# Performance work log

Hardware: AMD Instinct MI355X
Metric: run time of the kernel (lower is better)

## Reference

```python
import jax, jax.numpy as jnp
import numpy as np

SIZE = 128
DELTA = 1.0
NUM_SHELLS = SIZE // 2  # 64 shells up to Nyquist; corners beyond Nyquist are discarded
DROP_DC = False
ALPHA = None
EPS = 1e-8


def _make_shell_idx(n, delta):
    # integer-frequency radial coordinate, same grid as torch.fft.fftfreq(n)*n
    f = np.fft.fftfreq(n) * n
    fx, fy, fz = np.meshgrid(f, f, f, indexing="ij")
    r = np.sqrt(fx * fx + fy * fy + fz * fz)
    idx = np.floor(r / delta).astype(np.int32)
    # voxels past the Nyquist shell go to a discard bucket (index NUM_SHELLS)
    idx = np.where(idx < NUM_SHELLS, idx, NUM_SHELLS)
    return idx


def setup_inputs() -> dict:
    key = jax.random.key(0)
    k1, k2 = jax.random.split(key)
    shape = (8, 1, SIZE, SIZE, SIZE)
    img_ref = jax.random.normal(k1, shape, dtype=jnp.float32)
    img_pred = jax.random.normal(k2, shape, dtype=jnp.float32)
    shell_idx = jnp.asarray(_make_shell_idx(SIZE, DELTA))
    return {"img_ref": img_ref, "img_pred": img_pred, "shell_idx": shell_idx}


def reference(img_ref, img_pred, shell_idx):
    B = img_ref.shape[0] * img_ref.shape[1]
    V = SIZE * SIZE * SIZE
    F1 = jnp.fft.fftn(img_ref, axes=(-3, -2, -1)).reshape(B, V)
    F2 = jnp.fft.fftn(img_pred, axes=(-3, -2, -1)).reshape(B, V)
    idx = shell_idx.reshape(V)

    # per-shell reductions (single pass, replaces num_shells dense mask-multiplies)
    cross = (F1 * jnp.conj(F2)).real          # Re sum F1 conj(F2) per shell
    p1 = (F1.real ** 2 + F1.imag ** 2)
    p2 = (F2.real ** 2 + F2.imag ** 2)

    seg = jax.vmap(lambda x: jax.ops.segment_sum(x, idx, num_segments=NUM_SHELLS + 1))
    num = seg(cross)[:, :NUM_SHELLS]          # [B, num_shells], drop discard bucket
    d1 = seg(p1)[:, :NUM_SHELLS]
    d2 = seg(p2)[:, :NUM_SHELLS]

    fsc = num / (jnp.sqrt(d1 * d2) + EPS)     # [B, num_shells]

    if ALPHA is not None:
        freq = (jnp.arange(NUM_SHELLS, dtype=jnp.float32) + 0.5) * DELTA / SIZE
        fsc = fsc * (freq ** ALPHA)
    if DROP_DC:
        fsc = fsc[:, 1:]

    loss = 1.0 - jnp.mean(fsc ** 2)
    return loss
```

## Files before the change

kernel.cpp:

```cpp
#include <hip/hip_runtime.h>
#include <math.h>

#define N      128
#define LOGN   7
#define NSQ    (N * N)
#define VOL    (N * N * N)
#define NSHELL 64
#define BTOT   8
#define FPI    3.14159265358979323846f

#define TL     16
#define TP     (TL + 1)

__device__ inline float2* fft16(float2* A, float2* B, int t) {
    const int j5 = t & 31;
    const int lg = (t >> 5) << 1;
    float2* src = A;
    float2* dst = B;
#pragma unroll
    for (int s = 0; s < 6; s += 2) {
        const int Ns = 1 << s;
        const int m  = j5 & (Ns - 1);
        const int cc = j5 >> s;
        const int e0 = (cc << (s + 2)) + m;
        float s2, c2;
        __sincosf(-FPI * (float)m / (float)(2 * Ns), &s2, &c2);
        const float cw = c2 * c2 - s2 * s2;
        const float sw = 2.f * c2 * s2;
        __syncthreads();
#pragma unroll
        for (int l = 0; l < 2; ++l) {
            const int line = lg + l;
            const float2 a  = src[ j5       * TP + line];
            const float2 cv = src[(j5 + 32) * TP + line];
            const float2 b  = src[(j5 + 64) * TP + line];
            const float2 d  = src[(j5 + 96) * TP + line];
            const float wbx = b.x * cw - b.y * sw, wby = b.x * sw + b.y * cw;
            const float wdx = d.x * cw - d.y * sw, wdy = d.x * sw + d.y * cw;
            const float Apx = a.x + wbx, Apy = a.y + wby;
            const float Amx = a.x - wbx, Amy = a.y - wby;
            const float Bpx = cv.x + wdx, Bpy = cv.y + wdy;
            const float Bmx = cv.x - wdx, Bmy = cv.y - wdy;
            const float t0x = Bpx * c2 - Bpy * s2, t0y = Bpx * s2 + Bpy * c2;
            const float t1x = Bmx * c2 - Bmy * s2, t1y = Bmx * s2 + Bmy * c2;
            dst[(e0)          * TP + line] = make_float2(Apx + t0x, Apy + t0y);
            dst[(e0 + Ns)     * TP + line] = make_float2(Amx + t1y, Amy - t1x);
            dst[(e0 + 2 * Ns) * TP + line] = make_float2(Apx - t0x, Apy - t0y);
            dst[(e0 + 3 * Ns) * TP + line] = make_float2(Amx - t1y, Amy + t1x);
        }
        float2* tmp = src; src = dst; dst = tmp;
    }
    {
        const int m   = t & 63;
        const int grp = (t >> 6) << 2;
        float sw, cw;
        __sincosf(-FPI * (float)m / 64.f, &sw, &cw);
        __syncthreads();
#pragma unroll
        for (int l = 0; l < 4; ++l) {
            const int line = grp + l;
            const float2 v0 = src[m * TP + line];
            const float2 v1 = src[(m + 64) * TP + line];
            const float wx = v1.x * cw - v1.y * sw;
            const float wy = v1.x * sw + v1.y * cw;
            dst[m * TP + line]        = make_float2(v0.x + wx, v0.y + wy);
            dst[(m + 64) * TP + line] = make_float2(v0.x - wx, v0.y - wy);
        }
    }
    __syncthreads();
    return dst;
}

__global__ __launch_bounds__(256) void k_fftz_pack(const float* __restrict__ ref,
                                                   const float* __restrict__ pred,
                                                   float2* __restrict__ Z, int b0) {
    __shared__ float2 A[N * TP], B[N * TP];
    const int t  = threadIdx.x;
    const int yt = blockIdx.x & 7;
    const int x  = (blockIdx.x >> 3) & (N - 1);
    const int bl = blockIdx.x >> 10;
    const size_t inbase = (size_t)(b0 + bl) * VOL + (size_t)x * NSQ + (size_t)yt * TL * N;
    const size_t zbase  = (size_t)bl * VOL + (size_t)x * NSQ + (size_t)yt * TL * N;
#pragma unroll
    for (int i = 0; i < 8; ++i) {
        const int elem = i * 256 + t;
        const int z = elem & (N - 1);
        const int j = elem >> LOGN;
        A[z * TP + j] = make_float2(ref[inbase + elem], pred[inbase + elem]);
    }
    float2* res = fft16(A, B, t);
#pragma unroll
    for (int i = 0; i < 8; ++i) {
        const int elem = i * 256 + t;
        const int z = elem & (N - 1);
        const int j = elem >> LOGN;
        Z[zbase + elem] = res[z * TP + j];
    }
}

__global__ __launch_bounds__(256) void k_fft_strided(float2* __restrict__ Z,
                                                     int stride, int midmul) {
    __shared__ float2 A[N * TP], B[N * TP];
    const int t   = threadIdx.x;
    const int zt  = blockIdx.x & 7;
    const int mid = (blockIdx.x >> 3) & (N - 1);
    const int bl  = blockIdx.x >> 10;
    const size_t base = (size_t)bl * VOL + (size_t)mid * midmul + (size_t)zt * TL;
#pragma unroll
    for (int i = 0; i < 8; ++i) {
        const int elem = i * 256 + t;
        const int zz = elem & (TL - 1);
        const int j  = elem >> 4;
        A[j * TP + zz] = Z[base + (size_t)j * stride + zz];
    }
    float2* res = fft16(A, B, t);
#pragma unroll
    for (int i = 0; i < 8; ++i) {
        const int elem = i * 256 + t;
        const int zz = elem & (TL - 1);
        const int j  = elem >> 4;
        Z[base + (size_t)j * stride + zz] = res[j * TP + zz];
    }
}

__device__ inline int isqrt_i(int r2) {
    int s = (int)sqrtf((float)r2);
    s -= (s * s > r2);
    s += ((s + 1) * (s + 1) <= r2);
    return s;
}

__global__ __launch_bounds__(256) void k_reduce(const float2* __restrict__ Z,
                                                float* __restrict__ accum, int b0) {
    const int tid = threadIdx.x;
    const int bl  = blockIdx.x >> 9;
    const int x   = (blockIdx.x >> 2) & (N - 1);
    const int y0  = (blockIdx.x & 3) * 16;
    const int z   = tid & (N - 1);
    const int ys  = (tid >> 7) * 8;

    const int fx = x - ((x >= 64) ? N : 0);
    const int fz = z - ((z >= 64) ? N : 0);

    if (fx * fx + y0 * y0 >= 4096) return;

    __shared__ float sh[4 * 193];
    for (int i = tid; i < 4 * 193; i += 256) sh[i] = 0.f;
    __syncthreads();

    const int mx = (N - x) & (N - 1);
    const int mz = (N - z) & (N - 1);
    const size_t zb = (size_t)bl * VOL;
    const float2* Ap = Z + zb + (size_t)x  * NSQ + z;
    const float2* Bp = Z + zb + (size_t)mx * NSQ + mz;

    float* bins = sh + (tid & 3) * 193;
    const int fxx = fx * fx;
    const int fzz = fz * fz;

    float aC = 0.f, aP1 = 0.f, aP2 = 0.f;
    int cs = -1;
#pragma unroll
    for (int j = 0; j < 8; ++j) {
        const int y  = y0 + ys + j;
        const int s  = isqrt_i(fxx + y * y + fzz);
        if (s != cs) {
            if (cs >= 0 && cs < NSHELL) {
                atomicAdd(&bins[cs * 3 + 0], aC);
                atomicAdd(&bins[cs * 3 + 1], aP1);
                atomicAdd(&bins[cs * 3 + 2], aP2);
            }
            cs = s; aC = 0.f; aP1 = 0.f; aP2 = 0.f;
        }
        if (s < NSHELL) {
            const float w = (y == 0) ? 1.f : 2.f;
            const int my = (N - y) & (N - 1);
            const float2 Av = Ap[(size_t)y  * N];
            const float2 Bv = Bp[(size_t)my * N];
            const float F1x = 0.5f * (Av.x + Bv.x);
            const float F1y = 0.5f * (Av.y - Bv.y);
            const float F2x = 0.5f * (Av.y + Bv.y);
            const float F2y = 0.5f * (Bv.x - Av.x);
            aC  += w * (F1x * F2x + F1y * F2y);
            aP1 += w * (F1x * F1x + F1y * F1y);
            aP2 += w * (F2x * F2x + F2y * F2y);
        }
    }
    if (cs >= 0 && cs < NSHELL) {
        atomicAdd(&bins[cs * 3 + 0], aC);
        atomicAdd(&bins[cs * 3 + 1], aP1);
        atomicAdd(&bins[cs * 3 + 2], aP2);
    }
    __syncthreads();

    float* acc = accum + (size_t)(b0 + bl) * (NSHELL * 3);
    for (int i = tid; i < NSHELL * 3; i += 256) {
        const float v = sh[i] + sh[193 + i] + sh[2 * 193 + i] + sh[3 * 193 + i];
        atomicAdd(&acc[i], v);
    }
}

__global__ __launch_bounds__(512) void k_final(const float* __restrict__ accum,
                                               float* __restrict__ out) {
    __shared__ float red[8];
    const int tid = threadIdx.x;
    const float* a = accum + (size_t)tid * 3;
    const float fsc = a[0] / (sqrtf(a[1] * a[2]) + 1e-8f);
    float v = fsc * fsc;
#pragma unroll
    for (int off = 32; off > 0; off >>= 1) v += __shfl_down(v, off);
    if ((tid & 63) == 0) red[tid >> 6] = v;
    __syncthreads();
    if (tid == 0) {
        float ssum = 0.f;
#pragma unroll
        for (int i = 0; i < 8; ++i) ssum += red[i];
        out[0] = 1.0f - ssum / 512.0f;
    }
}

extern "C" void kernel_launch(void* const* d_in, const int* in_sizes, int n_in,
                              void* d_out, int out_size, void* d_ws, size_t ws_size,
                              hipStream_t stream) {
    const float* ref  = (const float*)d_in[0];
    const float* pred = (const float*)d_in[1];
    float* out = (float*)d_out;

    char*   ws    = (char*)d_ws;
    float*  accum = (float*)ws;
    float2* Zbuf  = (float2*)(ws + 8192);

    const size_t zbytes = (size_t)VOL * sizeof(float2);
    int cap = 1;
    if (ws_size > 8192) {
        size_t c = (ws_size - 8192) / zbytes;
        cap = (c < 1) ? 1 : (c > BTOT ? BTOT : (int)c);
    }

    hipMemsetAsync(accum, 0, BTOT * NSHELL * 3 * sizeof(float), stream);

    for (int b0 = 0; b0 < BTOT; b0 += cap) {
        const int nb = (BTOT - b0 < cap) ? (BTOT - b0) : cap;
        const int nblk = nb * 1024;
        k_fftz_pack<<<nblk, 256, 0, stream>>>(ref, pred, Zbuf, b0);
        k_fft_strided<<<nblk, 256, 0, stream>>>(Zbuf, N, NSQ);
        k_fft_strided<<<nblk, 256, 0, stream>>>(Zbuf, NSQ, N);
        k_reduce<<<nb * 512, 256, 0, stream>>>(Zbuf, accum, b0);
    }
    k_final<<<1, 512, 0, stream>>>(accum, out);
}
```

Baseline: 309.4 us.

## Fuse z/y FFTs per plane and x-FFT into shell reduction using wave shuffles

Replaces the shared-memory radix-4 FFT pipeline (three FFT kernels plus a reduction kernel) with two kernels. The first does the z and y FFTs of a whole x-plane, using wavefront shuffle-based 128-point FFTs with bit-reversed stores through an on-chip plane buffer. The second does the x-axis FFT and the shell reduction together, with no intermediate global write. This removes two full read/write passes over the complex volume and the extra launches. In exchange it needs large shared-memory tiles and 1024-thread blocks, and it reorganises the symmetry handling (full y range, no weight factor), which lowers occupancy and changes the amount of reduction work.

```diff
diff --git a/kernel.cpp b/kernel.cpp
--- a/kernel.cpp
+++ b/kernel.cpp
@@ -2,124 +2,83 @@
 #include <math.h>
 
 #define N      128
-#define LOGN   7
 #define NSQ    (N * N)
 #define VOL    (N * N * N)
 #define NSHELL 64
 #define BTOT   8
 #define FPI    3.14159265358979323846f
 
-#define TL     16
-#define TP     (TL + 1)
-
-__device__ inline float2* fft16(float2* A, float2* B, int t) {
-    const int j5 = t & 31;
-    const int lg = (t >> 5) << 1;
-    float2* src = A;
-    float2* dst = B;
-#pragma unroll
-    for (int s = 0; s < 6; s += 2) {
-        const int Ns = 1 << s;
-        const int m  = j5 & (Ns - 1);
-        const int cc = j5 >> s;
-        const int e0 = (cc << (s + 2)) + m;
-        float s2, c2;
-        __sincosf(-FPI * (float)m / (float)(2 * Ns), &s2, &c2);
-        const float cw = c2 * c2 - s2 * s2;
-        const float sw = 2.f * c2 * s2;
-        __syncthreads();
-#pragma unroll
-        for (int l = 0; l < 2; ++l) {
-            const int line = lg + l;
-            const float2 a  = src[ j5       * TP + line];
-            const float2 cv = src[(j5 + 32) * TP + line];
-            const float2 b  = src[(j5 + 64) * TP + line];
-            const float2 d  = src[(j5 + 96) * TP + line];
-            const float wbx = b.x * cw - b.y * sw, wby = b.x * sw + b.y * cw;
-            const float wdx = d.x * cw - d.y * sw, wdy = d.x * sw + d.y * cw;
-            const float Apx = a.x + wbx, Apy = a.y + wby;
-            const float Amx = a.x - wbx, Amy = a.y - wby;
-            const float Bpx = cv.x + wdx, Bpy = cv.y + wdy;
-            const float Bmx = cv.x - wdx, Bmy = cv.y - wdy;
-            const float t0x = Bpx * c2 - Bpy * s2, t0y = Bpx * s2 + Bpy * c2;
-            const float t1x = Bmx * c2 - Bmy * s2, t1y = Bmx * s2 + Bmy * c2;
-            dst[(e0)          * TP + line] = make_float2(Apx + t0x, Apy + t0y);
-            dst[(e0 + Ns)     * TP + line] = make_float2(Amx + t1y, Amy - t1x);
-            dst[(e0 + 2 * Ns) * TP + line] = make_float2(Apx - t0x, Apy - t0y);
-            dst[(e0 + 3 * Ns) * TP + line] = make_float2(Amx - t1y, Amy + t1x);
-        }
-        float2* tmp = src; src = dst; dst = tmp;
-    }
+#define PP     130
+#define TP2    17
+
+__device__ inline void mk_tw(int l, float* tc, float* ts, float* te) {
+    __sincosf(-FPI * (float)l * (1.0f / 64.0f), &ts[0], &tc[0]);
+#pragma unroll
+    for (int k = 1; k <= 6; ++k) {
+        const int h = 64 >> k;
+        float s, c;
+        __sincosf(-FPI * (float)(l & (h - 1)) / (float)h, &s, &c);
+        const bool hi = (l & h) != 0;
+        tc[k] = hi ? c : 1.0f;
+        ts[k] = hi ? s : 0.0f;
+        te[k] = hi ? -1.0f : 1.0f;
+    }
+}
+
+__device__ inline void fft128(float2& v0, float2& v1,
+                              const float* tc, const float* ts, const float* te) {
     {
-        const int m   = t & 63;
-        const int grp = (t >> 6) << 2;
-        float sw, cw;
-        __sincosf(-FPI * (float)m / 64.f, &sw, &cw);
-        __syncthreads();
-#pragma unroll
-        for (int l = 0; l < 4; ++l) {
-            const int line = grp + l;
-            const float2 v0 = src[m * TP + line];
-            const float2 v1 = src[(m + 64) * TP + line];
-            const float wx = v1.x * cw - v1.y * sw;
-            const float wy = v1.x * sw + v1.y * cw;
-            dst[m * TP + line]        = make_float2(v0.x + wx, v0.y + wy);
-            dst[(m + 64) * TP + line] = make_float2(v0.x - wx, v0.y - wy);
-        }
-    }
-    __syncthreads();
-    return dst;
-}
-
-__global__ __launch_bounds__(256) void k_fftz_pack(const float* __restrict__ ref,
-                                                   const float* __restrict__ pred,
-                                                   float2* __restrict__ Z, int b0) {
-    __shared__ float2 A[N * TP], B[N * TP];
-    const int t  = threadIdx.x;
-    const int yt = blockIdx.x & 7;
-    const int x  = (blockIdx.x >> 3) & (N - 1);
-    const int bl = blockIdx.x >> 10;
-    const size_t inbase = (size_t)(b0 + bl) * VOL + (size_t)x * NSQ + (size_t)yt * TL * N;
-    const size_t zbase  = (size_t)bl * VOL + (size_t)x * NSQ + (size_t)yt * TL * N;
-#pragma unroll
-    for (int i = 0; i < 8; ++i) {
-        const int elem = i * 256 + t;
-        const int z = elem & (N - 1);
-        const int j = elem >> LOGN;
-        A[z * TP + j] = make_float2(ref[inbase + elem], pred[inbase + elem]);
-    }
-    float2* res = fft16(A, B, t);
-#pragma unroll
-    for (int i = 0; i < 8; ++i) {
-        const int elem = i * 256 + t;
-        const int z = elem & (N - 1);
-        const int j = elem >> LOGN;
-        Z[zbase + elem] = res[z * TP + j];
-    }
-}
-
-__global__ __launch_bounds__(256) void k_fft_strided(float2* __restrict__ Z,
-                                                     int stride, int midmul) {
-    __shared__ float2 A[N * TP], B[N * TP];
-    const int t   = threadIdx.x;
-    const int zt  = blockIdx.x & 7;
-    const int mid = (blockIdx.x >> 3) & (N - 1);
-    const int bl  = blockIdx.x >> 10;
-    const size_t base = (size_t)bl * VOL + (size_t)mid * midmul + (size_t)zt * TL;
-#pragma unroll
-    for (int i = 0; i < 8; ++i) {
-        const int elem = i * 256 + t;
-        const int zz = elem & (TL - 1);
-        const int j  = elem >> 4;
-        A[j * TP + zz] = Z[base + (size_t)j * stride + zz];
-    }
-    float2* res = fft16(A, B, t);
-#pragma unroll
-    for (int i = 0; i < 8; ++i) {
-        const int elem = i * 256 + t;
-        const int zz = elem & (TL - 1);
-        const int j  = elem >> 4;
-        Z[base + (size_t)j * stride + zz] = res[j * TP + zz];
+        const float dx = v0.x - v1.x, dy = v0.y - v1.y;
+        v0.x += v1.x; v0.y += v1.y;
+        v1.x = dx * tc[0] - dy * ts[0];
+        v1.y = dx * ts[0] + dy * tc[0];
+    }
+#pragma unroll
+    for (int k = 1; k <= 6; ++k) {
+        const int h = 64 >> k;
+        const float c = tc[k], s = ts[k], e = te[k];
+        const float o0x = __shfl_xor(v0.x, h), o0y = __shfl_xor(v0.y, h);
+        const float o1x = __shfl_xor(v1.x, h), o1y = __shfl_xor(v1.y, h);
+        const float t0x = fmaf(e, v0.x, o0x), t0y = fmaf(e, v0.y, o0y);
+        const float t1x = fmaf(e, v1.x, o1x), t1y = fmaf(e, v1.y, o1y);
+        v0.x = t0x * c - t0y * s;  v0.y = t0x * s + t0y * c;
+        v1.x = t1x * c - t1y * s;  v1.y = t1x * s + t1y * c;
+    }
+}
+
+__global__ __launch_bounds__(1024) void k_fft_zy(const float* __restrict__ ref,
+                                                 const float* __restrict__ pred,
+                                                 float2* __restrict__ Z, int b0) {
+    __shared__ __align__(16) float2 plane[N * PP];
+    const int t = threadIdx.x, l = t & 63, w = t >> 6;
+    const int x  = blockIdx.x & (N - 1);
+    const int bl = blockIdx.x >> 7;
+    float tc[7], ts[7], te[7];
+    mk_tw(l, tc, ts, te);
+    const int f2 = (int)(__brev((unsigned)l) >> 26) << 1;
+
+    const size_t inb = (size_t)(b0 + bl) * VOL + (size_t)x * NSQ;
+#pragma unroll 2
+    for (int k = 0; k < 8; ++k) {
+        const int y = w * 8 + k;
+        const float* rp = ref  + inb + (size_t)y * N;
+        const float* pp = pred + inb + (size_t)y * N;
+        float2 v0 = make_float2(rp[l],      pp[l]);
+        float2 v1 = make_float2(rp[l + 64], pp[l + 64]);
+        fft128(v0, v1, tc, ts, te);
+        *reinterpret_cast<float4*>(&plane[y * PP + f2]) =
+            make_float4(v0.x, v0.y, v1.x, v1.y);
+    }
+    __syncthreads();
+    const size_t zb = (size_t)bl * VOL + (size_t)x * NSQ;
+#pragma unroll 2
+    for (int k = 0; k < 8; ++k) {
+        const int z = w * 8 + k;
+        float2 v0 = plane[l * PP + z];
+        float2 v1 = plane[(l + 64) * PP + z];
+        fft128(v0, v1, tc, ts, te);
+        *reinterpret_cast<float4*>(&Z[zb + (size_t)z * N + f2]) =
+            make_float4(v0.x, v0.y, v1.x, v1.y);
     }
 }
 
@@ -130,72 +89,96 @@
     return s;
 }
 
-__global__ __launch_bounds__(256) void k_reduce(const float2* __restrict__ Z,
-                                                float* __restrict__ accum, int b0) {
-    const int tid = threadIdx.x;
-    const int bl  = blockIdx.x >> 9;
-    const int x   = (blockIdx.x >> 2) & (N - 1);
-    const int y0  = (blockIdx.x & 3) * 16;
-    const int z   = tid & (N - 1);
-    const int ys  = (tid >> 7) * 8;
-
+__global__ __launch_bounds__(512, 4) void k_fftx_reduce(const float2* __restrict__ Z,
+                                                        float* __restrict__ accum, int b0) {
+    const int t = threadIdx.x, l = t & 63, w = t >> 6;
+    const int yt = blockIdx.x & 7;
+    const int z  = (blockIdx.x >> 3) & (N - 1);
+    const int bl = blockIdx.x >> 10;
+    const int fz = z - ((z >= 64) ? N : 0);
+    const int minfy = (yt < 4) ? yt * 16 : 113 - yt * 16;
+    if (fz * fz + minfy * minfy >= NSHELL * NSHELL) return;
+
+    __shared__ __align__(16) float2 TT[2 * N * TP2];
+    __shared__ float bins[4 * 193];
+    const int NT = N * TP2;
+
+    const int mz = (N - z) & (N - 1);
+    const size_t zbA = (size_t)bl * VOL + (size_t)z  * N;
+    const size_t zbB = (size_t)bl * VOL + (size_t)mz * N;
+#pragma unroll
+    for (int k = 0; k < 4; ++k) {
+        const int e  = k * 512 + t;
+        const int xx = e >> 4, yi = e & 15;
+        const int y  = yt * 16 + yi;
+        const int my = (N - y) & (N - 1);
+        TT[xx * TP2 + yi]      = Z[zbA + (size_t)xx * NSQ + y];
+        TT[NT + xx * TP2 + yi] = Z[zbB + (size_t)xx * NSQ + my];
+    }
+    for (int i = t; i < 4 * 193; i += 512) bins[i] = 0.f;
+
+    float tc[7], ts[7], te[7];
+    mk_tw(l, tc, ts, te);
+    const int f2 = (int)(__brev((unsigned)l) >> 26) << 1;
+    __syncthreads();
+
+#pragma unroll
+    for (int k = 0; k < 4; ++k) {
+        const int idx = w * 4 + k;
+        float2* T = TT + (idx >> 4) * NT;
+        const int i = idx & 15;
+        float2 v0 = T[l * TP2 + i];
+        float2 v1 = T[(l + 64) * TP2 + i];
+        fft128(v0, v1, tc, ts, te);
+        T[f2 * TP2 + i]       = v0;
+        T[(f2 + 1) * TP2 + i] = v1;
+    }
+    __syncthreads();
+
+    float* mybins = bins + (t & 3) * 193;
+    const int x  = t & (N - 1);
+    const int ih = t >> 7;
+    const int mx = (N - x) & (N - 1);
     const int fx = x - ((x >= 64) ? N : 0);
-    const int fz = z - ((z >= 64) ? N : 0);
-
-    if (fx * fx + y0 * y0 >= 4096) return;
-
-    __shared__ float sh[4 * 193];
-    for (int i = tid; i < 4 * 193; i += 256) sh[i] = 0.f;
-    __syncthreads();
-
-    const int mx = (N - x) & (N - 1);
-    const int mz = (N - z) & (N - 1);
-    const size_t zb = (size_t)bl * VOL;
-    const float2* Ap = Z + zb + (size_t)x  * NSQ + z;
-    const float2* Bp = Z + zb + (size_t)mx * NSQ + mz;
-
-    float* bins = sh + (tid & 3) * 193;
-    const int fxx = fx * fx;
-    const int fzz = fz * fz;
-
+    const int fxz = fx * fx + fz * fz;
     float aC = 0.f, aP1 = 0.f, aP2 = 0.f;
     int cs = -1;
 #pragma unroll
-    for (int j = 0; j < 8; ++j) {
-        const int y  = y0 + ys + j;
-        const int s  = isqrt_i(fxx + y * y + fzz);
+    for (int j = 0; j < 4; ++j) {
+        const int yi = ih * 4 + j;
+        const int y  = yt * 16 + yi;
+        const int fy = y - ((y >= 64) ? N : 0);
+        const int s  = isqrt_i(fxz + fy * fy);
         if (s != cs) {
             if (cs >= 0 && cs < NSHELL) {
-                atomicAdd(&bins[cs * 3 + 0], aC);
-                atomicAdd(&bins[cs * 3 + 1], aP1);
-                atomicAdd(&bins[cs * 3 + 2], aP2);
+                atomicAdd(&mybins[cs * 3 + 0], aC);
+                atomicAdd(&mybins[cs * 3 + 1], aP1);
+                atomicAdd(&mybins[cs * 3 + 2], aP2);
             }
             cs = s; aC = 0.f; aP1 = 0.f; aP2 = 0.f;
         }
         if (s < NSHELL) {
-            const float w = (y == 0) ? 1.f : 2.f;
-            const int my = (N - y) & (N - 1);
-            const float2 Av = Ap[(size_t)y  * N];
-            const float2 Bv = Bp[(size_t)my * N];
+            const float2 Av = TT[x * TP2 + yi];
+            const float2 Bv = TT[NT + mx * TP2 + yi];
             const float F1x = 0.5f * (Av.x + Bv.x);
             const float F1y = 0.5f * (Av.y - Bv.y);
             const float F2x = 0.5f * (Av.y + Bv.y);
             const float F2y = 0.5f * (Bv.x - Av.x);
-            aC  += w * (F1x * F2x + F1y * F2y);
-            aP1 += w * (F1x * F1x + F1y * F1y);
-            aP2 += w * (F2x * F2x + F2y * F2y);
+            aC  += F1x * F2x + F1y * F2y;
+            aP1 += F1x * F1x + F1y * F1y;
+            aP2 += F2x * F2x + F2y * F2y;
         }
     }
     if (cs >= 0 && cs < NSHELL) {
-        atomicAdd(&bins[cs * 3 + 0], aC);
-        atomicAdd(&bins[cs * 3 + 1], aP1);
-        atomicAdd(&bins[cs * 3 + 2], aP2);
+        atomicAdd(&mybins[cs * 3 + 0], aC);
+        atomicAdd(&mybins[cs * 3 + 1], aP1);
+        atomicAdd(&mybins[cs * 3 + 2], aP2);
     }
     __syncthreads();
 
     float* acc = accum + (size_t)(b0 + bl) * (NSHELL * 3);
-    for (int i = tid; i < NSHELL * 3; i += 256) {
-        const float v = sh[i] + sh[193 + i] + sh[2 * 193 + i] + sh[3 * 193 + i];
+    for (int i = t; i < NSHELL * 3; i += 512) {
+        const float v = bins[i] + bins[193 + i] + bins[2 * 193 + i] + bins[3 * 193 + i];
         atomicAdd(&acc[i], v);
     }
 }
@@ -241,11 +224,8 @@
 
     for (int b0 = 0; b0 < BTOT; b0 += cap) {
         const int nb = (BTOT - b0 < cap) ? (BTOT - b0) : cap;
-        const int nblk = nb * 1024;
-        k_fftz_pack<<<nblk, 256, 0, stream>>>(ref, pred, Zbuf, b0);
-        k_fft_strided<<<nblk, 256, 0, stream>>>(Zbuf, N, NSQ);
-        k_fft_strided<<<nblk, 256, 0, stream>>>(Zbuf, NSQ, N);
-        k_reduce<<<nb * 512, 256, 0, stream>>>(Zbuf, accum, b0);
+        k_fft_zy<<<nb * 128, 1024, 0, stream>>>(ref, pred, Zbuf, b0);
+        k_fftx_reduce<<<nb * 1024, 512, 0, stream>>>(Zbuf, accum, b0);
     }
     k_final<<<1, 512, 0, stream>>>(accum, out);
 }
```

Result: slower. 419.1 us (+35.4%).
